# Kernel tuning notes

Measured on AMD Instinct MI355X. Metric: run time of the kernel, lower is better.

The kernel has to match this reference:

```python
import jax, jax.numpy as jnp
import numpy as np

C_PARAM = 2.0
EPS = 1e-05

def setup_inputs() -> dict:
    key = jax.random.key(0)
    x = jax.random.normal(key, (2048, 512, 7, 7), dtype=jnp.float32)
    return {"x": x}

def reference(x) -> jnp.ndarray:
    # y[n,c] = spatial mean over HW
    y = jnp.mean(x, axis=(2, 3))                      # [N, C]
    # per-sample channel stats (biased variance, matching mean(x^2)-mean^2)
    m = jnp.mean(y, axis=1, keepdims=True)            # [N, 1]
    mx2 = jnp.mean(y * y, axis=1, keepdims=True)      # [N, 1]
    var = jnp.maximum(mx2 - m * m, 0.0)
    inv_std = jax.lax.rsqrt(var + EPS)
    y_norm = (y - m) * inv_std                        # [N, C]
    gate = jnp.exp(-0.5 * C_PARAM * y_norm * y_norm)  # [N, C]
    return x * gate[:, :, None, None]
```

## Files before the change

kernel.cpp:

```cpp
#include <hip/hip_runtime.h>
#include <hip/hip_bf16.h>
#include <math.h>


#define NN 2048
#define CC 512
#define HW 49
#define EPS 1e-5f

__global__ __launch_bounds__(512) void gate_kernel(const float* __restrict__ x,
                                                   float* __restrict__ out) {
    const int n = blockIdx.x;
    const int c = threadIdx.x;

    const size_t base = ((size_t)n * CC + c) * HW;
    const float* xp = x + base;

    float v[HW];
    float s = 0.0f;
#pragma unroll
    for (int i = 0; i < HW; ++i) {
        v[i] = xp[i];
        s += v[i];
    }
    const float y = s * (1.0f / (float)HW);

    float sum = y;
    float sum2 = y * y;
#pragma unroll
    for (int off = 32; off > 0; off >>= 1) {
        sum  += __shfl_down(sum, off);
        sum2 += __shfl_down(sum2, off);
    }

    __shared__ float wsum[8];
    __shared__ float wsum2[8];
    const int wave = threadIdx.x >> 6;
    const int lane = threadIdx.x & 63;
    if (lane == 0) {
        wsum[wave] = sum;
        wsum2[wave] = sum2;
    }
    __syncthreads();

    __shared__ float s_m, s_inv;
    if (threadIdx.x == 0) {
        float ts = 0.0f, ts2 = 0.0f;
#pragma unroll
        for (int w = 0; w < 8; ++w) {
            ts += wsum[w];
            ts2 += wsum2[w];
        }
        const float m = ts * (1.0f / (float)CC);
        float var = ts2 * (1.0f / (float)CC) - m * m;
        var = fmaxf(var, 0.0f);
        s_m = m;
        s_inv = rsqrtf(var + EPS);
    }
    __syncthreads();

    const float yn = (y - s_m) * s_inv;
    const float gate = expf(-yn * yn);

    float* op = out + base;
#pragma unroll
    for (int i = 0; i < HW; ++i) {
        op[i] = v[i] * gate;
    }
}

extern "C" void kernel_launch(void* const* d_in, const int* in_sizes, int n_in,
                              void* d_out, int out_size, void* d_ws, size_t ws_size,
                              hipStream_t stream) {
    const float* x = (const float*)d_in[0];
    float* out = (float*)d_out;
    gate_kernel<<<NN, CC, 0, stream>>>(x, out);
}
```

Before: 366.7 us.

## Stage loads and stores through LDS in chunks for coalesced float4 access

Before this change each thread read and wrote its own channel's 49 contiguous floats, so neighbouring lanes hit addresses 196 bytes apart and global access was uncoalesced. The kernel now copies 128-channel chunks into shared memory with coalesced float4 loads, lets each thread pick up its channel's values from LDS, and does the mirror-image staging for the output. The cost is extra barriers and serialized chunk phases. Each thread also reads LDS at a 49-float stride, which may cause bank conflicts, and the ~25KB of LDS per block may limit occupancy.

New measurement: 346.0 us. -5.6%, faster.

```diff
diff --git a/kernel.cpp b/kernel.cpp
--- a/kernel.cpp
+++ b/kernel.cpp
@@ -1,56 +1,62 @@
 #include <hip/hip_runtime.h>
-#include <hip/hip_bf16.h>
 #include <math.h>
 
 
 #define NN 2048
 #define CC 512
 #define HW 49
+#define CHCH 128
+#define CHEL (CHCH * HW)
+#define CHV4 (CHEL / 4)
+#define NCHUNK (CC / CHCH)
 #define EPS 1e-5f
 
-__global__ __launch_bounds__(512) void gate_kernel(const float* __restrict__ x,
-                                                   float* __restrict__ out) {
+__global__ __launch_bounds__(512, 4) void gate_kernel(const float* __restrict__ x,
+                                                      float* __restrict__ out) {
+    __shared__ float lds[CHEL];
+    __shared__ float wsum[8];
+    __shared__ float wsum2[8];
+    __shared__ float s_m, s_inv;
+
     const int n = blockIdx.x;
-    const int c = threadIdx.x;
-
-    const size_t base = ((size_t)n * CC + c) * HW;
-    const float* xp = x + base;
+    const int tid = threadIdx.x;
+    const size_t nbase = (size_t)n * (CC * HW);
 
     float v[HW];
+
+    const float4* __restrict__ xin4 = (const float4*)(x + nbase);
+    for (int j = 0; j < NCHUNK; ++j) {
+        for (int i = tid; i < CHV4; i += 512) {
+            ((float4*)lds)[i] = xin4[j * CHV4 + i];
+        }
+        __syncthreads();
+        if ((tid >> 7) == j) {
+            const int base = (tid & (CHCH - 1)) * HW;
+#pragma unroll
+            for (int l = 0; l < HW; ++l) v[l] = lds[base + l];
+        }
+        __syncthreads();
+    }
+
     float s = 0.0f;
 #pragma unroll
-    for (int i = 0; i < HW; ++i) {
-        v[i] = xp[i];
-        s += v[i];
-    }
+    for (int l = 0; l < HW; ++l) s += v[l];
     const float y = s * (1.0f / (float)HW);
 
-    float sum = y;
-    float sum2 = y * y;
+    float sum = y, sum2 = y * y;
 #pragma unroll
     for (int off = 32; off > 0; off >>= 1) {
         sum  += __shfl_down(sum, off);
         sum2 += __shfl_down(sum2, off);
     }
-
-    __shared__ float wsum[8];
-    __shared__ float wsum2[8];
-    const int wave = threadIdx.x >> 6;
-    const int lane = threadIdx.x & 63;
-    if (lane == 0) {
-        wsum[wave] = sum;
-        wsum2[wave] = sum2;
-    }
+    const int wave = tid >> 6;
+    const int lane = tid & 63;
+    if (lane == 0) { wsum[wave] = sum; wsum2[wave] = sum2; }
     __syncthreads();
-
-    __shared__ float s_m, s_inv;
-    if (threadIdx.x == 0) {
+    if (tid == 0) {
         float ts = 0.0f, ts2 = 0.0f;
 #pragma unroll
-        for (int w = 0; w < 8; ++w) {
-            ts += wsum[w];
-            ts2 += wsum2[w];
-        }
+        for (int w = 0; w < 8; ++w) { ts += wsum[w]; ts2 += wsum2[w]; }
         const float m = ts * (1.0f / (float)CC);
         float var = ts2 * (1.0f / (float)CC) - m * m;
         var = fmaxf(var, 0.0f);
@@ -62,10 +68,18 @@
     const float yn = (y - s_m) * s_inv;
     const float gate = expf(-yn * yn);
 
-    float* op = out + base;
+    float4* __restrict__ out4 = (float4*)(out + nbase);
+    for (int j = 0; j < NCHUNK; ++j) {
+        if ((tid >> 7) == j) {
+            const int base = (tid & (CHCH - 1)) * HW;
 #pragma unroll
-    for (int i = 0; i < HW; ++i) {
-        op[i] = v[i] * gate;
+            for (int l = 0; l < HW; ++l) lds[base + l] = v[l] * gate;
+        }
+        __syncthreads();
+        for (int i = tid; i < CHV4; i += 512) {
+            out4[j * CHV4 + i] = ((float4*)lds)[i];
+        }
+        __syncthreads();
     }
 }
 
@@ -74,5 +88,5 @@
                               hipStream_t stream) {
     const float* x = (const float*)d_in[0];
     float* out = (float*)d_out;
-    gate_kernel<<<NN, CC, 0, stream>>>(x, out);
+    gate_kernel<<<NN, 512, 0, stream>>>(x, out);
 }
```
